# Performance work log

Measured on AMD Instinct MI355X. Metric: run time of the kernel, lower is better.

Reference implementation:

```python
import jax, jax.numpy as jnp
import numpy as np

B, T, C = 1, 4096, 1024
H = 16
D = C // H  # head_dim = 64


def setup_inputs() -> dict:
    key = jax.random.key(0)
    ks = jax.random.split(key, 9)
    s = 1.0 / np.sqrt(C)
    return {
        "x": jax.random.normal(ks[0], (B, T, C), dtype=jnp.float32),
        "Wq": jax.random.normal(ks[1], (C, C), dtype=jnp.float32) * s,
        "bq": jnp.zeros((C,), dtype=jnp.float32),
        "Wk": jax.random.normal(ks[2], (C, C), dtype=jnp.float32) * s,
        "bk": jnp.zeros((C,), dtype=jnp.float32),
        "Wv": jax.random.normal(ks[3], (C, C), dtype=jnp.float32) * s,
        "bv": jnp.zeros((C,), dtype=jnp.float32),
        "Wo": jax.random.normal(ks[4], (C, C), dtype=jnp.float32) * s,
        "bo": jnp.zeros((C,), dtype=jnp.float32),
    }


def reference(x, Wq, bq, Wk, bk, Wv, bv, Wo, bo):
    # QKV projections (torch Linear: y = x @ W.T + b)
    q = x @ Wq.T + bq
    k = x @ Wk.T + bk
    v = x @ Wv.T + bv
    # [B,T,C] -> [B,H,T,D]
    q = q.reshape(B, T, H, D).transpose(0, 2, 1, 3)
    k = k.reshape(B, T, H, D).transpose(0, 2, 1, 3)
    v = v.reshape(B, T, H, D).transpose(0, 2, 1, 3)
    scale = 1.0 / jnp.sqrt(jnp.asarray(D, dtype=q.dtype))
    scores = jnp.einsum("bhqd,bhkd->bhqk", q, k) * scale  # [B,H,T,T]
    attn = jax.nn.softmax(scores, axis=-1)
    out = jnp.einsum("bhqk,bhkd->bhqd", attn, v)  # [B,H,T,D]
    out = out.transpose(0, 2, 1, 3).reshape(B, T, C)
    return out @ Wo.T + bo
```

## Files before the change

kernel.cpp:

```cpp
#include <hip/hip_runtime.h>
#include <stdint.h>

#define T_SEQ 4096
#define CDIM  1024
#define NH    16
#define DH    64

typedef _Float16 half8 __attribute__((ext_vector_type(8)));
typedef _Float16 half4 __attribute__((ext_vector_type(4)));
typedef float    f32x4 __attribute__((ext_vector_type(4)));

#if __has_builtin(__builtin_amdgcn_exp2f)
#define EXP2F(x) __builtin_amdgcn_exp2f(x)
#else
#define EXP2F(x) exp2f(x)
#endif

#define MFMA_K32(a, b, c) __builtin_amdgcn_mfma_f32_16x16x32_f16(a, b, c, 0, 0, 0)

__device__ __forceinline__ void gl_lds16(const void* g, void* l) {
  __builtin_amdgcn_global_load_lds(
      (const __attribute__((address_space(1))) uint32_t*)g,
      (__attribute__((address_space(3))) uint32_t*)l, 16, 0, 0);
}

__global__ void cvt_all_kernel(const float* __restrict__ w0, const float* __restrict__ w1,
                               const float* __restrict__ w2, const float* __restrict__ w3,
                               const float* __restrict__ x,
                               _Float16* __restrict__ o0, _Float16* __restrict__ o1,
                               _Float16* __restrict__ o2, _Float16* __restrict__ o3,
                               _Float16* __restrict__ xo) {
  int y = blockIdx.y;
  const float* src;
  _Float16* dst;
  if (y < 4) {
    src = (y == 0) ? w0 : (y == 1) ? w1 : (y == 2) ? w2 : w3;
    dst = (y == 0) ? o0 : (y == 1) ? o1 : (y == 2) ? o2 : o3;
  } else {
    src = x  + (size_t)(y - 4) * (CDIM * CDIM);
    dst = xo + (size_t)(y - 4) * (CDIM * CDIM);
  }
  int i = (blockIdx.x * blockDim.x + threadIdx.x) * 8;
  float4 f0 = *(const float4*)(src + i);
  float4 f1 = *(const float4*)(src + i + 4);
  half8 h = { (_Float16)f0.x, (_Float16)f0.y, (_Float16)f0.z, (_Float16)f0.w,
              (_Float16)f1.x, (_Float16)f1.y, (_Float16)f1.z, (_Float16)f1.w };
  *(half8*)(dst + i) = h;
}

__device__ __forceinline__ void gemm_core(const _Float16* __restrict__ A,
                                          const _Float16* __restrict__ Bm,
                                          _Float16* As, _Float16* Bs,
                                          int bm, int bn,
                                          f32x4 (&acc)[4][4]) {
  const int tid  = threadIdx.x;
  const int lane = tid & 63;
  const int wave = tid >> 6;
  const int waveM = wave >> 1, waveN = wave & 1;
  const int quad = lane >> 4, c16 = lane & 15;

  const int rs0 = wave * 32 + (lane >> 2);
  const int rs1 = rs0 + 16;
  const int dm0 = ((lane & 3) ^ ((rs0 >> 1) & 3)) * 8;
  const int dm1 = ((lane & 3) ^ ((rs1 >> 1) & 3)) * 8;

  const _Float16* gA0 = A  + (size_t)(bm * 128 + rs0) * CDIM + dm0;
  const _Float16* gA1 = A  + (size_t)(bm * 128 + rs1) * CDIM + dm1;
  const _Float16* gB0 = Bm + (size_t)(bn * 128 + rs0) * CDIM + dm0;
  const _Float16* gB1 = Bm + (size_t)(bn * 128 + rs1) * CDIM + dm1;
  _Float16* lA0 = As + wave * 1024;
  _Float16* lA1 = lA0 + 512;
  _Float16* lB0 = Bs + wave * 1024;
  _Float16* lB1 = lB0 + 512;

  const int xsw  = (c16 >> 1) & 3;
  const int offA = (waveM * 64 + c16) * 32 + ((quad ^ xsw) * 8);
  const int offB = (waveN * 64 + c16) * 32 + ((quad ^ xsw) * 8);

  for (int kk = 0; kk < 32; ++kk) {
    gl_lds16(gA0, lA0);
    gl_lds16(gA1, lA1);
    gl_lds16(gB0, lB0);
    gl_lds16(gB1, lB1);
    __syncthreads();
    half8 a[4], b[4];
#pragma unroll
    for (int i = 0; i < 4; ++i) a[i] = *(const half8*)(As + offA + i * 512);
#pragma unroll
    for (int i = 0; i < 4; ++i) b[i] = *(const half8*)(Bs + offB + i * 512);
#pragma unroll
    for (int mi = 0; mi < 4; ++mi)
#pragma unroll
      for (int ni = 0; ni < 4; ++ni)
        acc[mi][ni] = MFMA_K32(a[mi], b[ni], acc[mi][ni]);
    gA0 += 32; gA1 += 32; gB0 += 32; gB1 += 32;
    __syncthreads();
  }
}

__device__ __forceinline__ void gemm_core64(const _Float16* __restrict__ A,
                                            const _Float16* __restrict__ Bm,
                                            _Float16* As, _Float16* Bs,
                                            int bm, int bn,
                                            f32x4 (&acc)[2][4]) {
  const int tid  = threadIdx.x;
  const int lane = tid & 63;
  const int wave = tid >> 6;
  const int waveM = wave >> 1, waveN = wave & 1;
  const int quad = lane >> 4, c16 = lane & 15;

  const int rsA = wave * 16 + (lane >> 2);
  const int dmA = ((lane & 3) ^ ((rsA >> 1) & 3)) * 8;
  const int rs0 = wave * 32 + (lane >> 2);
  const int rs1 = rs0 + 16;
  const int dm0 = ((lane & 3) ^ ((rs0 >> 1) & 3)) * 8;
  const int dm1 = ((lane & 3) ^ ((rs1 >> 1) & 3)) * 8;

  const _Float16* gA0 = A  + (size_t)(bm * 64  + rsA) * CDIM + dmA;
  const _Float16* gB0 = Bm + (size_t)(bn * 128 + rs0) * CDIM + dm0;
  const _Float16* gB1 = Bm + (size_t)(bn * 128 + rs1) * CDIM + dm1;
  _Float16* lA0 = As + wave * 512;
  _Float16* lB0 = Bs + wave * 1024;
  _Float16* lB1 = lB0 + 512;

  const int xsw  = (c16 >> 1) & 3;
  const int offA = (waveM * 32 + c16) * 32 + ((quad ^ xsw) * 8);
  const int offB = (waveN * 64 + c16) * 32 + ((quad ^ xsw) * 8);

  for (int kk = 0; kk < 32; ++kk) {
    gl_lds16(gA0, lA0);
    gl_lds16(gB0, lB0);
    gl_lds16(gB1, lB1);
    __syncthreads();
    half8 a[2], b[4];
#pragma unroll
    for (int i = 0; i < 2; ++i) a[i] = *(const half8*)(As + offA + i * 512);
#pragma unroll
    for (int i = 0; i < 4; ++i) b[i] = *(const half8*)(Bs + offB + i * 512);
#pragma unroll
    for (int mi = 0; mi < 2; ++mi)
#pragma unroll
      for (int ni = 0; ni < 4; ++ni)
        acc[mi][ni] = MFMA_K32(a[mi], b[ni], acc[mi][ni]);
    gA0 += 32; gB0 += 32; gB1 += 32;
    __syncthreads();
  }
}

__global__ __launch_bounds__(256) void qkv_gemm(
    const _Float16* __restrict__ xh,
    const _Float16* __restrict__ wqh, const _Float16* __restrict__ wkh, const _Float16* __restrict__ wvh,
    const float* __restrict__ bq, const float* __restrict__ bk, const float* __restrict__ bv,
    _Float16* __restrict__ qh, _Float16* __restrict__ kh, _Float16* __restrict__ vth) {
  __shared__ __align__(16) _Float16 As[128 * 32];
  __shared__ __align__(16) _Float16 Bs[128 * 32];
  const int z = blockIdx.z;
  const _Float16* W   = (z == 0) ? wqh : ((z == 1) ? wkh : wvh);
  const float*    bias = (z == 0) ? bq  : ((z == 1) ? bk  : bv);

  f32x4 acc[4][4];
  const f32x4 zf = {0.f, 0.f, 0.f, 0.f};
#pragma unroll
  for (int i = 0; i < 4; ++i)
#pragma unroll
    for (int j = 0; j < 4; ++j) acc[i][j] = zf;

  gemm_core(xh, W, As, Bs, blockIdx.x, blockIdx.y, acc);

  const int lane = threadIdx.x & 63, wave = threadIdx.x >> 6;
  const int waveM = wave >> 1, waveN = wave & 1;
  const int quad = lane >> 4, c16 = lane & 15;
  const int rowb = blockIdx.x * 128 + waveM * 64;
  const int colb = blockIdx.y * 128 + waveN * 64;

  float bsv[4];
#pragma unroll
  for (int ni = 0; ni < 4; ++ni) bsv[ni] = bias[colb + ni * 16 + c16];

  if (z < 2) {
    _Float16* outp = (z == 0) ? qh : kh;
    const float scl = (z == 0) ? 0.18033688011112042f : 1.0f;
#pragma unroll
    for (int mi = 0; mi < 4; ++mi)
#pragma unroll
      for (int ni = 0; ni < 4; ++ni) {
        int col = colb + ni * 16 + c16;
        int hh = col >> 6, dd = col & 63;
#pragma unroll
        for (int r = 0; r < 4; ++r) {
          int row = rowb + mi * 16 + quad * 4 + r;
          outp[(size_t)(hh * T_SEQ + row) * DH + dd] = (_Float16)((acc[mi][ni][r] + bsv[ni]) * scl);
        }
      }
  } else {
#pragma unroll
    for (int mi = 0; mi < 4; ++mi)
#pragma unroll
      for (int ni = 0; ni < 4; ++ni) {
        int col  = colb + ni * 16 + c16;
        int row0 = rowb + mi * 16 + quad * 4;
        half4 h4;
#pragma unroll
        for (int r = 0; r < 4; ++r) h4[r] = (_Float16)(acc[mi][ni][r] + bsv[ni]);
        *(half4*)(vth + (size_t)col * T_SEQ + row0) = h4;
      }
  }
}

__global__ __launch_bounds__(256) void out_gemm(
    const _Float16* __restrict__ ctx, const _Float16* __restrict__ woh,
    const float* __restrict__ bo, float* __restrict__ out) {
  __shared__ __align__(16) _Float16 As[64 * 32];
  __shared__ __align__(16) _Float16 Bs[128 * 32];
  f32x4 acc[2][4];
  const f32x4 zf = {0.f, 0.f, 0.f, 0.f};
#pragma unroll
  for (int i = 0; i < 2; ++i)
#pragma unroll
    for (int j = 0; j < 4; ++j) acc[i][j] = zf;

  gemm_core64(ctx, woh, As, Bs, blockIdx.x, blockIdx.y, acc);

  const int lane = threadIdx.x & 63, wave = threadIdx.x >> 6;
  const int waveM = wave >> 1, waveN = wave & 1;
  const int quad = lane >> 4, c16 = lane & 15;
  const int rowb = blockIdx.x * 64 + waveM * 32;
  const int colb = blockIdx.y * 128 + waveN * 64;

  float bsv[4];
#pragma unroll
  for (int ni = 0; ni < 4; ++ni) bsv[ni] = bo[colb + ni * 16 + c16];

#pragma unroll
  for (int mi = 0; mi < 2; ++mi)
#pragma unroll
    for (int ni = 0; ni < 4; ++ni) {
      int col = colb + ni * 16 + c16;
#pragma unroll
      for (int r = 0; r < 4; ++r) {
        int row = rowb + mi * 16 + quad * 4 + r;
        out[(size_t)row * CDIM + col] = acc[mi][ni][r] + bsv[ni];
      }
    }
}

__global__ __launch_bounds__(256, 2) void attn_kernel(
    const _Float16* __restrict__ qh, const _Float16* __restrict__ kh,
    const _Float16* __restrict__ vth, _Float16* __restrict__ ctx) {
  __shared__ __align__(16) _Float16 Ks[2][64 * 64];
  __shared__ __align__(16) _Float16 Vs[2][64 * 64];
  __shared__ __align__(16) _Float16 Ps[4][32 * 64];

  const int tid = threadIdx.x, lane = tid & 63, wave = tid >> 6;
  const int quad = lane >> 4, c16 = lane & 15;
  const int h = blockIdx.y;
  const int qw = blockIdx.x * 128 + wave * 32;

  half8 qf[2][2];
#pragma unroll
  for (int qg = 0; qg < 2; ++qg)
#pragma unroll
    for (int c = 0; c < 2; ++c)
      qf[qg][c] = *(const half8*)(qh + (size_t)(h * T_SEQ + qw + qg * 16 + c16) * DH + c * 32 + quad * 8);

  const int rs0 = wave * 16 + (lane >> 3);
  const int rs1 = rs0 + 8;
  const int dm0 = ((lane & 7) ^ (rs0 & 7)) * 8;
  const int dm1 = ((lane & 7) ^ (rs1 & 7)) * 8;
  const _Float16* gK0 = kh  + (size_t)(h * T_SEQ + rs0) * DH + dm0;
  const _Float16* gK1 = kh  + (size_t)(h * T_SEQ + rs1) * DH + dm1;
  const _Float16* gV0 = vth + (size_t)(h * DH + rs0) * T_SEQ + dm0;
  const _Float16* gV1 = vth + (size_t)(h * DH + rs1) * T_SEQ + dm1;
  const int lo0 = wave * 1024, lo1 = wave * 1024 + 512;

  _Float16* Pw = &Ps[wave][0];

  f32x4 o[2][4];
  f32x4 lacc[2];
  const f32x4 zf = {0.f, 0.f, 0.f, 0.f};
#pragma unroll
  for (int qg = 0; qg < 2; ++qg) {
#pragma unroll
    for (int db = 0; db < 4; ++db) o[qg][db] = zf;
    lacc[qg] = zf;
  }
  const half8 ones8 = { (_Float16)1, (_Float16)1, (_Float16)1, (_Float16)1,
                        (_Float16)1, (_Float16)1, (_Float16)1, (_Float16)1 };

  gl_lds16(gK0, &Ks[0][lo0]);
  gl_lds16(gK1, &Ks[0][lo1]);
  gl_lds16(gV0, &Vs[0][lo0]);
  gl_lds16(gV1, &Vs[0][lo1]);
  gK0 += 64 * DH; gK1 += 64 * DH; gV0 += 64; gV1 += 64;
  __syncthreads();

  auto step = [&](int bc, int bn, bool pf) {
    if (pf) {
      gl_lds16(gK0, &Ks[bn][lo0]);
      gl_lds16(gK1, &Ks[bn][lo1]);
      gl_lds16(gV0, &Vs[bn][lo0]);
      gl_lds16(gV1, &Vs[bn][lo1]);
      gK0 += 64 * DH; gK1 += 64 * DH; gV0 += 64; gV1 += 64;
    }
    const _Float16* Kb = &Ks[bc][0];
    const _Float16* Vb = &Vs[bc][0];

    const f32x4 minit = {-16.f, -16.f, -16.f, -16.f};
    f32x4 s[2][4];
#pragma unroll
    for (int qg = 0; qg < 2; ++qg)
#pragma unroll
      for (int kb = 0; kb < 4; ++kb) s[qg][kb] = minit;
#pragma unroll
    for (int c = 0; c < 2; ++c) {
#pragma unroll
      for (int kb = 0; kb < 4; ++kb) {
        int key = kb * 16 + c16;
        half8 ak = *(const half8*)(Kb + key * 64 + (((c * 4 + quad) ^ (key & 7)) * 8));
        s[0][kb] = MFMA_K32(ak, qf[0][c], s[0][kb]);
        s[1][kb] = MFMA_K32(ak, qf[1][c], s[1][kb]);
      }
    }

#pragma unroll
    for (int qg = 0; qg < 2; ++qg) {
#pragma unroll
      for (int kb = 0; kb < 4; ++kb) {
        half4 pk;
#pragma unroll
        for (int r = 0; r < 4; ++r) pk[r] = (_Float16)EXP2F(s[qg][kb][r]);
        int row = qg * 16 + c16;
        int g   = kb * 2 + (quad >> 1);
        *(half4*)(Pw + row * 64 + ((g ^ (row & 7)) * 8) + (quad & 1) * 4) = pk;
      }
    }

    half8 av[2][4];
#pragma unroll
    for (int kb32 = 0; kb32 < 2; ++kb32)
#pragma unroll
      for (int db = 0; db < 4; ++db) {
        int d = db * 16 + c16;
        av[kb32][db] = *(const half8*)(Vb + d * 64 + (((kb32 * 4 + quad) ^ (d & 7)) * 8));
      }

#pragma unroll
    for (int qg = 0; qg < 2; ++qg) {
      int row = qg * 16 + c16;
#pragma unroll
      for (int kb32 = 0; kb32 < 2; ++kb32) {
        half8 bp = *(const half8*)(Pw + row * 64 + (((kb32 * 4 + quad) ^ (row & 7)) * 8));
        lacc[qg] = MFMA_K32(ones8, bp, lacc[qg]);
#pragma unroll
        for (int db = 0; db < 4; ++db)
          o[qg][db] = MFMA_K32(av[kb32][db], bp, o[qg][db]);
      }
    }
  };

  for (int it = 0; it < 32; ++it) {
    step(0, 1, true);
    __syncthreads();
    step(1, 0, it < 31);
    __syncthreads();
  }

#pragma unroll
  for (int qg = 0; qg < 2; ++qg) {
    float inv = 1.f / lacc[qg][0];
#pragma unroll
    for (int db = 0; db < 4; ++db) {
      half4 h4;
#pragma unroll
      for (int r = 0; r < 4; ++r) h4[r] = (_Float16)(o[qg][db][r] * inv);
      int row = qg * 16 + c16;
      int g   = db * 2 + (quad >> 1);
      *(half4*)(Pw + row * 64 + ((g ^ (row & 7)) * 8) + (quad & 1) * 4) = h4;
    }
  }
  const int q = lane >> 1, hv = lane & 1;
#pragma unroll
  for (int i = 0; i < 4; ++i) {
    int g = hv * 4 + i;
    half8 vv = *(const half8*)(Pw + q * 64 + ((g ^ (q & 7)) * 8));
    *(half8*)(ctx + (size_t)(qw + q) * CDIM + h * DH + g * 8) = vv;
  }
}

extern "C" void kernel_launch(void* const* d_in, const int* in_sizes, int n_in,
                              void* d_out, int out_size, void* d_ws, size_t ws_size,
                              hipStream_t stream) {
  const float* x  = (const float*)d_in[0];
  const float* Wq = (const float*)d_in[1];
  const float* bq = (const float*)d_in[2];
  const float* Wk = (const float*)d_in[3];
  const float* bk = (const float*)d_in[4];
  const float* Wv = (const float*)d_in[5];
  const float* bv = (const float*)d_in[6];
  const float* Wo = (const float*)d_in[7];
  const float* bo = (const float*)d_in[8];
  float* out = (float*)d_out;

  char* ws = (char*)d_ws;
  _Float16* xh  = (_Float16*)(ws);
  _Float16* qh  = (_Float16*)(ws + ((size_t)8  << 20));
  _Float16* kh  = (_Float16*)(ws + ((size_t)16 << 20));
  _Float16* vth = (_Float16*)(ws + ((size_t)24 << 20));
  _Float16* wqh = (_Float16*)(ws + ((size_t)32 << 20));
  _Float16* wkh = (_Float16*)(ws + ((size_t)34 << 20));
  _Float16* wvh = (_Float16*)(ws + ((size_t)36 << 20));
  _Float16* woh = (_Float16*)(ws + ((size_t)38 << 20));
  _Float16* ctx = xh;

  cvt_all_kernel<<<dim3(512, 8), 256, 0, stream>>>(Wq, Wk, Wv, Wo, x,
                                                   wqh, wkh, wvh, woh, xh);
  qkv_gemm<<<dim3(32, 8, 3), 256, 0, stream>>>(xh, wqh, wkh, wvh, bq, bk, bv, qh, kh, vth);
  attn_kernel<<<dim3(32, 16), 256, 0, stream>>>(qh, kh, vth, ctx);
  out_gemm<<<dim3(64, 8), 256, 0, stream>>>(ctx, woh, bo, out);
}
```

Measured before the change: 223.9 us.

## Split attention over two key halves, merging with atomics and a normalize kernel

The attention grid gains a z dimension, so each block processes half of the key sequence. The unnormalized outputs are merged with fp16 half2 atomic adds and the row sums with fp32 atomics; a new kernel then divides by the sum and writes the context. Occupancy is raised from 2 to 3 blocks per CU. The aim is more parallel work per CU to hide latency, paid for by two memsets, an extra kernel launch, atomic traffic, and the precision risk of accumulating unnormalized partial outputs in fp16.

```diff
diff --git a/kernel.cpp b/kernel.cpp
--- a/kernel.cpp
+++ b/kernel.cpp
@@ -1,4 +1,5 @@
 #include <hip/hip_runtime.h>
+#include <hip/hip_fp16.h>
 #include <stdint.h>
 
 #define T_SEQ 4096
@@ -244,9 +245,10 @@
     }
 }
 
-__global__ __launch_bounds__(256, 2) void attn_kernel(
+__global__ __launch_bounds__(256, 3) void attn_kernel(
     const _Float16* __restrict__ qh, const _Float16* __restrict__ kh,
-    const _Float16* __restrict__ vth, _Float16* __restrict__ ctx) {
+    const _Float16* __restrict__ vth, _Float16* __restrict__ Oacc,
+    float* __restrict__ lg) {
   __shared__ __align__(16) _Float16 Ks[2][64 * 64];
   __shared__ __align__(16) _Float16 Vs[2][64 * 64];
   __shared__ __align__(16) _Float16 Ps[4][32 * 64];
@@ -254,7 +256,9 @@
   const int tid = threadIdx.x, lane = tid & 63, wave = tid >> 6;
   const int quad = lane >> 4, c16 = lane & 15;
   const int h = blockIdx.y;
+  const int z = blockIdx.z;
   const int qw = blockIdx.x * 128 + wave * 32;
+  const int k0 = z * (T_SEQ / 2);
 
   half8 qf[2][2];
 #pragma unroll
@@ -267,10 +271,10 @@
   const int rs1 = rs0 + 8;
   const int dm0 = ((lane & 7) ^ (rs0 & 7)) * 8;
   const int dm1 = ((lane & 7) ^ (rs1 & 7)) * 8;
-  const _Float16* gK0 = kh  + (size_t)(h * T_SEQ + rs0) * DH + dm0;
-  const _Float16* gK1 = kh  + (size_t)(h * T_SEQ + rs1) * DH + dm1;
-  const _Float16* gV0 = vth + (size_t)(h * DH + rs0) * T_SEQ + dm0;
-  const _Float16* gV1 = vth + (size_t)(h * DH + rs1) * T_SEQ + dm1;
+  const _Float16* gK0 = kh  + (size_t)(h * T_SEQ + k0 + rs0) * DH + dm0;
+  const _Float16* gK1 = kh  + (size_t)(h * T_SEQ + k0 + rs1) * DH + dm1;
+  const _Float16* gV0 = vth + (size_t)(h * DH + rs0) * T_SEQ + k0 + dm0;
+  const _Float16* gV1 = vth + (size_t)(h * DH + rs1) * T_SEQ + k0 + dm1;
   const int lo0 = wave * 1024, lo1 = wave * 1024 + 512;
 
   _Float16* Pw = &Ps[wave][0];
@@ -358,33 +362,46 @@
     }
   };
 
-  for (int it = 0; it < 32; ++it) {
+  for (int it = 0; it < 16; ++it) {
     step(0, 1, true);
     __syncthreads();
-    step(1, 0, it < 31);
-    __syncthreads();
-  }
-
-#pragma unroll
-  for (int qg = 0; qg < 2; ++qg) {
-    float inv = 1.f / lacc[qg][0];
-#pragma unroll
-    for (int db = 0; db < 4; ++db) {
-      half4 h4;
-#pragma unroll
-      for (int r = 0; r < 4; ++r) h4[r] = (_Float16)(o[qg][db][r] * inv);
-      int row = qg * 16 + c16;
-      int g   = db * 2 + (quad >> 1);
-      *(half4*)(Pw + row * 64 + ((g ^ (row & 7)) * 8) + (quad & 1) * 4) = h4;
-    }
-  }
-  const int q = lane >> 1, hv = lane & 1;
-#pragma unroll
-  for (int i = 0; i < 4; ++i) {
-    int g = hv * 4 + i;
-    half8 vv = *(const half8*)(Pw + q * 64 + ((g ^ (q & 7)) * 8));
-    *(half8*)(ctx + (size_t)(qw + q) * CDIM + h * DH + g * 8) = vv;
-  }
+    step(1, 0, it < 15);
+    __syncthreads();
+  }
+
+  {
+    __half2* ob = (__half2*)(Oacc + (size_t)h * T_SEQ * DH);
+#pragma unroll
+    for (int qg = 0; qg < 2; ++qg) {
+      int q = qw + qg * 16 + c16;
+#pragma unroll
+      for (int db = 0; db < 4; ++db) {
+#pragma unroll
+        for (int i = 0; i < 2; ++i) {
+          union { _Float16 e[2]; __half2 v; } u;
+          u.e[0] = (_Float16)o[qg][db][2 * i];
+          u.e[1] = (_Float16)o[qg][db][2 * i + 1];
+          unsafeAtomicAdd(ob + (size_t)q * 32 + db * 8 + quad * 2 + i, u.v);
+        }
+      }
+      if (quad == 0) unsafeAtomicAdd(lg + h * T_SEQ + q, lacc[qg][0]);
+    }
+  }
+}
+
+__global__ __launch_bounds__(256) void norm_kernel(const _Float16* __restrict__ Oacc,
+                                                   const float* __restrict__ lg,
+                                                   _Float16* __restrict__ ctx) {
+  int idx = blockIdx.x * blockDim.x + threadIdx.x;
+  int h  = idx >> 15;
+  int t  = (idx >> 3) & (T_SEQ - 1);
+  int dc = idx & 7;
+  float inv = 1.0f / lg[h * T_SEQ + t];
+  half8 v = *(const half8*)(Oacc + (size_t)idx * 8);
+  half8 r;
+#pragma unroll
+  for (int i = 0; i < 8; ++i) r[i] = (_Float16)((float)v[i] * inv);
+  *(half8*)(ctx + (size_t)t * CDIM + h * DH + dc * 8) = r;
 }
 
 extern "C" void kernel_launch(void* const* d_in, const int* in_sizes, int n_in,
@@ -402,19 +419,24 @@
   float* out = (float*)d_out;
 
   char* ws = (char*)d_ws;
-  _Float16* xh  = (_Float16*)(ws);
-  _Float16* qh  = (_Float16*)(ws + ((size_t)8  << 20));
-  _Float16* kh  = (_Float16*)(ws + ((size_t)16 << 20));
-  _Float16* vth = (_Float16*)(ws + ((size_t)24 << 20));
-  _Float16* wqh = (_Float16*)(ws + ((size_t)32 << 20));
-  _Float16* wkh = (_Float16*)(ws + ((size_t)34 << 20));
-  _Float16* wvh = (_Float16*)(ws + ((size_t)36 << 20));
-  _Float16* woh = (_Float16*)(ws + ((size_t)38 << 20));
-  _Float16* ctx = xh;
+  _Float16* xh   = (_Float16*)(ws);
+  _Float16* qh   = (_Float16*)(ws + ((size_t)8  << 20));
+  _Float16* kh   = (_Float16*)(ws + ((size_t)16 << 20));
+  _Float16* vth  = (_Float16*)(ws + ((size_t)24 << 20));
+  _Float16* wqh  = (_Float16*)(ws + ((size_t)32 << 20));
+  _Float16* wkh  = (_Float16*)(ws + ((size_t)34 << 20));
+  _Float16* wvh  = (_Float16*)(ws + ((size_t)36 << 20));
+  _Float16* woh  = (_Float16*)(ws + ((size_t)38 << 20));
+  _Float16* Oacc = xh;
+  float*    lg   = (float*)wqh;
+  _Float16* ctx  = kh;
 
   cvt_all_kernel<<<dim3(512, 8), 256, 0, stream>>>(Wq, Wk, Wv, Wo, x,
                                                    wqh, wkh, wvh, woh, xh);
   qkv_gemm<<<dim3(32, 8, 3), 256, 0, stream>>>(xh, wqh, wkh, wvh, bq, bk, bv, qh, kh, vth);
-  attn_kernel<<<dim3(32, 16), 256, 0, stream>>>(qh, kh, vth, ctx);
+  hipMemsetAsync(Oacc, 0, (size_t)NH * T_SEQ * DH * sizeof(_Float16), stream);
+  hipMemsetAsync(lg,   0, (size_t)NH * T_SEQ * sizeof(float), stream);
+  attn_kernel<<<dim3(32, 16, 2), 256, 0, stream>>>(qh, kh, vth, Oacc, lg);
+  norm_kernel<<<2048, 256, 0, stream>>>(Oacc, lg, ctx);
   out_gemm<<<dim3(64, 8), 256, 0, stream>>>(ctx, woh, bo, out);
 }
```

New measurement: 266.4 us. 1.19x slower.

## Double-buffer LDS in projection GEMMs and stage QKV epilogue through LDS

Applied to the files above, without the earlier changes.

Both the QKV and output projection GEMMs now use two LDS buffers. The next K-slice is prefetched with global_load_lds while the current one feeds MFMA, which drops one barrier per iteration and overlaps loads with compute. The QKV epilogue swaps the MFMA operands for Q/K so each lane holds contiguous head-dim values, then stages tiles in swizzled LDS and writes 16-byte coalesced stores in place of scattered 2-byte or 8-byte stores. LDS use per block doubles, which may lower occupancy.

```diff
diff --git a/kernel.cpp b/kernel.cpp
--- a/kernel.cpp
+++ b/kernel.cpp
@@ -48,11 +48,16 @@
   *(half8*)(dst + i) = h;
 }
 
-__device__ __forceinline__ void gemm_core(const _Float16* __restrict__ A,
-                                          const _Float16* __restrict__ Bm,
-                                          _Float16* As, _Float16* Bs,
-                                          int bm, int bn,
-                                          f32x4 (&acc)[4][4]) {
+__global__ __launch_bounds__(256) void qkv_gemm(
+    const _Float16* __restrict__ xh,
+    const _Float16* __restrict__ wqh, const _Float16* __restrict__ wkh, const _Float16* __restrict__ wvh,
+    const float* __restrict__ bq, const float* __restrict__ bk, const float* __restrict__ bv,
+    _Float16* __restrict__ qh, _Float16* __restrict__ kh, _Float16* __restrict__ vth) {
+  __shared__ __align__(16) _Float16 SM[16384];
+  const int z = blockIdx.z;
+  const _Float16* W    = (z == 0) ? wqh : ((z == 1) ? wkh : wvh);
+  const float*    bias = (z == 0) ? bq  : ((z == 1) ? bk  : bv);
+
   const int tid  = threadIdx.x;
   const int lane = tid & 63;
   const int wave = tid >> 6;
@@ -64,45 +69,139 @@
   const int dm0 = ((lane & 3) ^ ((rs0 >> 1) & 3)) * 8;
   const int dm1 = ((lane & 3) ^ ((rs1 >> 1) & 3)) * 8;
 
-  const _Float16* gA0 = A  + (size_t)(bm * 128 + rs0) * CDIM + dm0;
-  const _Float16* gA1 = A  + (size_t)(bm * 128 + rs1) * CDIM + dm1;
-  const _Float16* gB0 = Bm + (size_t)(bn * 128 + rs0) * CDIM + dm0;
-  const _Float16* gB1 = Bm + (size_t)(bn * 128 + rs1) * CDIM + dm1;
-  _Float16* lA0 = As + wave * 1024;
-  _Float16* lA1 = lA0 + 512;
-  _Float16* lB0 = Bs + wave * 1024;
-  _Float16* lB1 = lB0 + 512;
+  const _Float16* gA0 = xh + (size_t)(blockIdx.x * 128 + rs0) * CDIM + dm0;
+  const _Float16* gA1 = xh + (size_t)(blockIdx.x * 128 + rs1) * CDIM + dm1;
+  const _Float16* gB0 = W  + (size_t)(blockIdx.y * 128 + rs0) * CDIM + dm0;
+  const _Float16* gB1 = W  + (size_t)(blockIdx.y * 128 + rs1) * CDIM + dm1;
+  const int loA = wave * 1024;
+
+  f32x4 acc[4][4];
+  const f32x4 zf = {0.f, 0.f, 0.f, 0.f};
+#pragma unroll
+  for (int i = 0; i < 4; ++i)
+#pragma unroll
+    for (int j = 0; j < 4; ++j) acc[i][j] = zf;
 
   const int xsw  = (c16 >> 1) & 3;
   const int offA = (waveM * 64 + c16) * 32 + ((quad ^ xsw) * 8);
   const int offB = (waveN * 64 + c16) * 32 + ((quad ^ xsw) * 8);
-
-  for (int kk = 0; kk < 32; ++kk) {
-    gl_lds16(gA0, lA0);
-    gl_lds16(gA1, lA1);
-    gl_lds16(gB0, lB0);
-    gl_lds16(gB1, lB1);
-    __syncthreads();
+  const bool swap = (z < 2);
+
+  gl_lds16(gA0, SM + 0    + loA);
+  gl_lds16(gA1, SM + 0    + loA + 512);
+  gl_lds16(gB0, SM + 8192 + loA);
+  gl_lds16(gB1, SM + 8192 + loA + 512);
+  gA0 += 32; gA1 += 32; gB0 += 32; gB1 += 32;
+  __syncthreads();
+
+  auto step = [&](int bc, int bn, bool pf) {
+    if (pf) {
+      gl_lds16(gA0, SM + bn * 4096 + loA);
+      gl_lds16(gA1, SM + bn * 4096 + loA + 512);
+      gl_lds16(gB0, SM + 8192 + bn * 4096 + loA);
+      gl_lds16(gB1, SM + 8192 + bn * 4096 + loA + 512);
+      gA0 += 32; gA1 += 32; gB0 += 32; gB1 += 32;
+    }
+    const _Float16* Ab = SM + bc * 4096;
+    const _Float16* Bb = SM + 8192 + bc * 4096;
     half8 a[4], b[4];
 #pragma unroll
-    for (int i = 0; i < 4; ++i) a[i] = *(const half8*)(As + offA + i * 512);
-#pragma unroll
-    for (int i = 0; i < 4; ++i) b[i] = *(const half8*)(Bs + offB + i * 512);
-#pragma unroll
-    for (int mi = 0; mi < 4; ++mi)
-#pragma unroll
-      for (int ni = 0; ni < 4; ++ni)
-        acc[mi][ni] = MFMA_K32(a[mi], b[ni], acc[mi][ni]);
-    gA0 += 32; gA1 += 32; gB0 += 32; gB1 += 32;
-    __syncthreads();
-  }
-}
-
-__device__ __forceinline__ void gemm_core64(const _Float16* __restrict__ A,
-                                            const _Float16* __restrict__ Bm,
-                                            _Float16* As, _Float16* Bs,
-                                            int bm, int bn,
-                                            f32x4 (&acc)[2][4]) {
+    for (int i = 0; i < 4; ++i) a[i] = *(const half8*)(Ab + offA + i * 512);
+#pragma unroll
+    for (int i = 0; i < 4; ++i) b[i] = *(const half8*)(Bb + offB + i * 512);
+    if (swap) {
+#pragma unroll
+      for (int mi = 0; mi < 4; ++mi)
+#pragma unroll
+        for (int ni = 0; ni < 4; ++ni)
+          acc[mi][ni] = MFMA_K32(b[ni], a[mi], acc[mi][ni]);
+    } else {
+#pragma unroll
+      for (int mi = 0; mi < 4; ++mi)
+#pragma unroll
+        for (int ni = 0; ni < 4; ++ni)
+          acc[mi][ni] = MFMA_K32(a[mi], b[ni], acc[mi][ni]);
+    }
+  };
+
+  for (int it = 0; it < 16; ++it) {
+    step(0, 1, true);
+    __syncthreads();
+    step(1, 0, it < 15);
+    __syncthreads();
+  }
+
+  const int colb = blockIdx.y * 128 + waveN * 64;
+  const int rowb = blockIdx.x * 128 + waveM * 64;
+  const int hh   = colb >> 6;
+  _Float16* Ew = SM + wave * 4096;
+
+  if (z < 2) {
+    const float scl = (z == 0) ? 0.18033688011112042f : 1.0f;
+    float4 bs4[4];
+#pragma unroll
+    for (int ni = 0; ni < 4; ++ni)
+      bs4[ni] = *(const float4*)(bias + colb + ni * 16 + quad * 4);
+#pragma unroll
+    for (int mi = 0; mi < 4; ++mi) {
+      int t = mi * 16 + c16;
+#pragma unroll
+      for (int ni = 0; ni < 4; ++ni) {
+        int g = ni * 2 + (quad >> 1);
+        half4 h4 = { (_Float16)((acc[mi][ni][0] + bs4[ni].x) * scl),
+                     (_Float16)((acc[mi][ni][1] + bs4[ni].y) * scl),
+                     (_Float16)((acc[mi][ni][2] + bs4[ni].z) * scl),
+                     (_Float16)((acc[mi][ni][3] + bs4[ni].w) * scl) };
+        *(half4*)(Ew + t * 64 + ((g ^ (t & 7)) * 8) + (quad & 1) * 4) = h4;
+      }
+    }
+    _Float16* gbase = ((z == 0) ? qh : kh) + (size_t)hh * T_SEQ * DH + (size_t)rowb * DH;
+#pragma unroll
+    for (int hv2 = 0; hv2 < 2; ++hv2) {
+      int t = (lane >> 1) + hv2 * 32;
+#pragma unroll
+      for (int i = 0; i < 4; ++i) {
+        int g = (lane & 1) * 4 + i;
+        half8 v = *(const half8*)(Ew + t * 64 + ((g ^ (t & 7)) * 8));
+        *(half8*)(gbase + (size_t)t * DH + g * 8) = v;
+      }
+    }
+  } else {
+    float bsv[4];
+#pragma unroll
+    for (int ni = 0; ni < 4; ++ni) bsv[ni] = bias[colb + ni * 16 + c16];
+#pragma unroll
+    for (int ni = 0; ni < 4; ++ni) {
+      int d = ni * 16 + c16;
+#pragma unroll
+      for (int mi = 0; mi < 4; ++mi) {
+        int g = mi * 2 + (quad >> 1);
+        half4 h4;
+#pragma unroll
+        for (int r = 0; r < 4; ++r) h4[r] = (_Float16)(acc[mi][ni][r] + bsv[ni]);
+        *(half4*)(Ew + d * 64 + ((g ^ (d & 7)) * 8) + (quad & 1) * 4) = h4;
+      }
+    }
+    _Float16* gbase = vth + (size_t)hh * DH * T_SEQ + rowb;
+#pragma unroll
+    for (int hv2 = 0; hv2 < 2; ++hv2) {
+      int d = (lane >> 1) + hv2 * 32;
+#pragma unroll
+      for (int i = 0; i < 4; ++i) {
+        int g = (lane & 1) * 4 + i;
+        half8 v = *(const half8*)(Ew + d * 64 + ((g ^ (d & 7)) * 8));
+        *(half8*)(gbase + (size_t)d * T_SEQ + g * 8) = v;
+      }
+    }
+  }
+}
+
+__global__ __launch_bounds__(256) void out_gemm(
+    const _Float16* __restrict__ ctx, const _Float16* __restrict__ woh,
+    const float* __restrict__ bo, float* __restrict__ out) {
+  __shared__ __align__(16) _Float16 As[2][64 * 32];
+  __shared__ __align__(16) _Float16 Bs[2][128 * 32];
+
   const int tid  = threadIdx.x;
   const int lane = tid & 63;
   const int wave = tid >> 6;
@@ -116,114 +215,54 @@
   const int dm0 = ((lane & 3) ^ ((rs0 >> 1) & 3)) * 8;
   const int dm1 = ((lane & 3) ^ ((rs1 >> 1) & 3)) * 8;
 
-  const _Float16* gA0 = A  + (size_t)(bm * 64  + rsA) * CDIM + dmA;
-  const _Float16* gB0 = Bm + (size_t)(bn * 128 + rs0) * CDIM + dm0;
-  const _Float16* gB1 = Bm + (size_t)(bn * 128 + rs1) * CDIM + dm1;
-  _Float16* lA0 = As + wave * 512;
-  _Float16* lB0 = Bs + wave * 1024;
-  _Float16* lB1 = lB0 + 512;
+  const _Float16* gA0 = ctx + (size_t)(blockIdx.x * 64  + rsA) * CDIM + dmA;
+  const _Float16* gB0 = woh + (size_t)(blockIdx.y * 128 + rs0) * CDIM + dm0;
+  const _Float16* gB1 = woh + (size_t)(blockIdx.y * 128 + rs1) * CDIM + dm1;
+  const int loA = wave * 512, loB = wave * 1024;
+
+  f32x4 acc[2][4];
+  const f32x4 zf = {0.f, 0.f, 0.f, 0.f};
+#pragma unroll
+  for (int i = 0; i < 2; ++i)
+#pragma unroll
+    for (int j = 0; j < 4; ++j) acc[i][j] = zf;
 
   const int xsw  = (c16 >> 1) & 3;
   const int offA = (waveM * 32 + c16) * 32 + ((quad ^ xsw) * 8);
   const int offB = (waveN * 64 + c16) * 32 + ((quad ^ xsw) * 8);
 
-  for (int kk = 0; kk < 32; ++kk) {
-    gl_lds16(gA0, lA0);
-    gl_lds16(gB0, lB0);
-    gl_lds16(gB1, lB1);
-    __syncthreads();
+  gl_lds16(gA0, &As[0][loA]);
+  gl_lds16(gB0, &Bs[0][loB]);
+  gl_lds16(gB1, &Bs[0][loB + 512]);
+  gA0 += 32; gB0 += 32; gB1 += 32;
+  __syncthreads();
+
+  auto step = [&](int bc, int bn, bool pf) {
+    if (pf) {
+      gl_lds16(gA0, &As[bn][loA]);
+      gl_lds16(gB0, &Bs[bn][loB]);
+      gl_lds16(gB1, &Bs[bn][loB + 512]);
+      gA0 += 32; gB0 += 32; gB1 += 32;
+    }
     half8 a[2], b[4];
 #pragma unroll
-    for (int i = 0; i < 2; ++i) a[i] = *(const half8*)(As + offA + i * 512);
-#pragma unroll
-    for (int i = 0; i < 4; ++i) b[i] = *(const half8*)(Bs + offB + i * 512);
+    for (int i = 0; i < 2; ++i) a[i] = *(const half8*)(&As[bc][0] + offA + i * 512);
+#pragma unroll
+    for (int i = 0; i < 4; ++i) b[i] = *(const half8*)(&Bs[bc][0] + offB + i * 512);
 #pragma unroll
     for (int mi = 0; mi < 2; ++mi)
 #pragma unroll
       for (int ni = 0; ni < 4; ++ni)
         acc[mi][ni] = MFMA_K32(a[mi], b[ni], acc[mi][ni]);
-    gA0 += 32; gB0 += 32; gB1 += 32;
-    __syncthreads();
-  }
-}
-
-__global__ __launch_bounds__(256) void qkv_gemm(
-    const _Float16* __restrict__ xh,
-    const _Float16* __restrict__ wqh, const _Float16* __restrict__ wkh, const _Float16* __restrict__ wvh,
-    const float* __restrict__ bq, const float* __restrict__ bk, const float* __restrict__ bv,
-    _Float16* __restrict__ qh, _Float16* __restrict__ kh, _Float16* __restrict__ vth) {
-  __shared__ __align__(16) _Float16 As[128 * 32];
-  __shared__ __align__(16) _Float16 Bs[128 * 32];
-  const int z = blockIdx.z;
-  const _Float16* W   = (z == 0) ? wqh : ((z == 1) ? wkh : wvh);
-  const float*    bias = (z == 0) ? bq  : ((z == 1) ? bk  : bv);
-
-  f32x4 acc[4][4];
-  const f32x4 zf = {0.f, 0.f, 0.f, 0.f};
-#pragma unroll
-  for (int i = 0; i < 4; ++i)
-#pragma unroll
-    for (int j = 0; j < 4; ++j) acc[i][j] = zf;
-
-  gemm_core(xh, W, As, Bs, blockIdx.x, blockIdx.y, acc);
-
-  const int lane = threadIdx.x & 63, wave = threadIdx.x >> 6;
-  const int waveM = wave >> 1, waveN = wave & 1;
-  const int quad = lane >> 4, c16 = lane & 15;
-  const int rowb = blockIdx.x * 128 + waveM * 64;
-  const int colb = blockIdx.y * 128 + waveN * 64;
-
-  float bsv[4];
-#pragma unroll
-  for (int ni = 0; ni < 4; ++ni) bsv[ni] = bias[colb + ni * 16 + c16];
-
-  if (z < 2) {
-    _Float16* outp = (z == 0) ? qh : kh;
-    const float scl = (z == 0) ? 0.18033688011112042f : 1.0f;
-#pragma unroll
-    for (int mi = 0; mi < 4; ++mi)
-#pragma unroll
-      for (int ni = 0; ni < 4; ++ni) {
-        int col = colb + ni * 16 + c16;
-        int hh = col >> 6, dd = col & 63;
-#pragma unroll
-        for (int r = 0; r < 4; ++r) {
-          int row = rowb + mi * 16 + quad * 4 + r;
-          outp[(size_t)(hh * T_SEQ + row) * DH + dd] = (_Float16)((acc[mi][ni][r] + bsv[ni]) * scl);
-        }
-      }
-  } else {
-#pragma unroll
-    for (int mi = 0; mi < 4; ++mi)
-#pragma unroll
-      for (int ni = 0; ni < 4; ++ni) {
-        int col  = colb + ni * 16 + c16;
-        int row0 = rowb + mi * 16 + quad * 4;
-        half4 h4;
-#pragma unroll
-        for (int r = 0; r < 4; ++r) h4[r] = (_Float16)(acc[mi][ni][r] + bsv[ni]);
-        *(half4*)(vth + (size_t)col * T_SEQ + row0) = h4;
-      }
-  }
-}
-
-__global__ __launch_bounds__(256) void out_gemm(
-    const _Float16* __restrict__ ctx, const _Float16* __restrict__ woh,
-    const float* __restrict__ bo, float* __restrict__ out) {
-  __shared__ __align__(16) _Float16 As[64 * 32];
-  __shared__ __align__(16) _Float16 Bs[128 * 32];
-  f32x4 acc[2][4];
-  const f32x4 zf = {0.f, 0.f, 0.f, 0.f};
-#pragma unroll
-  for (int i = 0; i < 2; ++i)
-#pragma unroll
-    for (int j = 0; j < 4; ++j) acc[i][j] = zf;
-
-  gemm_core64(ctx, woh, As, Bs, blockIdx.x, blockIdx.y, acc);
-
-  const int lane = threadIdx.x & 63, wave = threadIdx.x >> 6;
-  const int waveM = wave >> 1, waveN = wave & 1;
-  const int quad = lane >> 4, c16 = lane & 15;
+  };
+
+  for (int it = 0; it < 16; ++it) {
+    step(0, 1, true);
+    __syncthreads();
+    step(1, 0, it < 15);
+    __syncthreads();
+  }
+
   const int rowb = blockIdx.x * 64 + waveM * 32;
   const int colb = blockIdx.y * 128 + waveN * 64;
 
```

After: 232.8 us. +4.0%, slower.
